# Kernel optimization log

Measured on AMD Instinct MI355X. Metric: run time of the kernel, lower is better.

Reference implementation:

```python
import jax, jax.numpy as jnp
import numpy as np

N, T, VN, C = 64, 512, 10, 128
HEADS, DH = 8, 16
INNER = HEADS * DH  # 128
BN_EPS = 1e-5


def _build_mask():
    # depth == 0 graph: facial-region connections + self links, symmetric 10x10
    m = np.zeros((VN, VN), dtype=np.float32)
    conn = [[0, 1], [0, 2], [2, 1], [3, 4], [3, 5], [4, 5],
            [6, 7], [6, 8], [6, 9], [8, 7], [9, 7], [8, 9]]
    for a, b in conn:
        m[a, b] = 1.0
        m[b, a] = 1.0
    for i in range(VN):
        m[i, i] = 1.0
    return jnp.asarray(m)


def setup_inputs() -> dict:
    key = jax.random.key(0)
    k = jax.random.split(key, 6)
    x = jax.random.normal(k[0], (N, T, VN, C), dtype=jnp.float32)
    gamma = 1.0 + 0.02 * jax.random.normal(k[1], (C,), dtype=jnp.float32)
    beta = 0.02 * jax.random.normal(k[2], (C,), dtype=jnp.float32)
    w_qkv = 0.02 * jax.random.normal(k[3], (C, 3 * INNER), dtype=jnp.float32)
    w_out = 0.02 * jax.random.normal(k[4], (INNER, C), dtype=jnp.float32)
    b_out = 0.02 * jax.random.normal(k[5], (C,), dtype=jnp.float32)
    return {"x": x, "gamma": gamma, "beta": beta, "w_qkv": w_qkv,
            "w_out": w_out, "b_out": b_out, "mask": _build_mask()}


def reference(x, gamma, beta, w_qkv, w_out, b_out, mask):
    n, t, vn, c = x.shape
    xb = x.reshape(-1, vn, c)                     # (b, vn, c), b = n*t
    # BatchNorm1d over channel c (training mode: batch stats over b and vn)
    mean = jnp.mean(xb, axis=(0, 1))
    var = jnp.var(xb, axis=(0, 1))                # biased, matches torch BN
    y = (xb - mean) * jax.lax.rsqrt(var + BN_EPS) * gamma + beta
    # fused QKV projection (Linear, no bias)
    qkv = y @ w_qkv                               # (b, vn, 3*inner)
    q, k, v = jnp.split(qkv, 3, axis=-1)
    split_heads = lambda z: z.reshape(-1, vn, HEADS, DH).transpose(0, 2, 1, 3)
    q, k, v = split_heads(q), split_heads(k), split_heads(v)  # (b, h, vn, dh)
    scale = DH ** -0.5
    dots = jnp.einsum('bhid,bhjd->bhij', q, k) * scale
    dots = dots * mask                            # multiplicative graph mask
    attn = jax.nn.softmax(dots, axis=-1)
    out = jnp.einsum('bhij,bhjd->bhid', attn, v)  # (b, h, vn, dh)
    out = out.transpose(0, 2, 1, 3).reshape(-1, vn, INNER)
    out = out @ w_out + b_out                     # output projection
    return out.reshape(n, t, vn, c)
```

## Files before the change

### kernel.cpp

```cpp
#include <hip/hip_runtime.h>


#define VNODES 10
#define CH 128
#define HEADS 8
#define ROWS_TOTAL 327680
#define G 8
#define MROWS 80
#define MT 5
#define SY 136
#define SQ 392

typedef __bf16 bf16x8 __attribute__((ext_vector_type(8)));
typedef float f32x4 __attribute__((ext_vector_type(4)));
typedef unsigned short u16x8 __attribute__((ext_vector_type(8)));
typedef unsigned short u16x4 __attribute__((ext_vector_type(4)));

__device__ __forceinline__ float bf2f(unsigned short u) {
    return __uint_as_float(((unsigned)u) << 16);
}
__device__ __forceinline__ unsigned short f2bf(float f) {
    unsigned u = __float_as_uint(f);
    u += 0x7fffu + ((u >> 16) & 1u);
    return (unsigned short)(u >> 16);
}

__global__ __launch_bounds__(256) void detect_kernel(
        const unsigned short* __restrict__ xr, int* __restrict__ flag) {
    __shared__ float red[256];
    int t = threadIdx.x;
    float mx = 0.f;
    for (int i = t; i < 8192; i += 256) {
        float a = fabsf(bf2f(xr[i]));
        if (!(a < 1e9f)) a = 1e9f;
        mx = fmaxf(mx, a);
    }
    red[t] = mx;
    __syncthreads();
    for (int s = 128; s > 0; s >>= 1) {
        if (t < s) red[t] = fmaxf(red[t], red[t + s]);
        __syncthreads();
    }
    if (t == 0) *flag = (red[0] > 1000.f) ? 1 : 0;
}

template<int MODE>
__global__ __launch_bounds__(256) void prep_kernel(
        const void* __restrict__ wqkv_, const void* __restrict__ wout_,
        const int* __restrict__ flag,
        unsigned short* __restrict__ fq, unsigned short* __restrict__ fo) {
    if (*flag != MODE) return;
    const unsigned short* wq16 = (const unsigned short*)wqkv_;
    const float*          wq32 = (const float*)wqkv_;
    const unsigned short* wo16 = (const unsigned short*)wout_;
    const float*          wo32 = (const float*)wout_;
    int tid = blockIdx.x * 256 + threadIdx.x;
    if (tid < 24 * 4 * 64) {
        int l = tid & 63;
        int kt = (tid >> 6) & 3;
        int nt = tid >> 8;
        int quad = l >> 4, n = l & 15;
#pragma unroll
        for (int j = 0; j < 8; ++j) {
            int idx = (kt * 32 + quad * 8 + j) * 384 + nt * 16 + n;
            fq[tid * 8 + j] = MODE ? f2bf(wq32[idx]) : wq16[idx];
        }
    } else if (tid < 24 * 4 * 64 + 8 * 4 * 64) {
        int u = tid - 24 * 4 * 64;
        int l = u & 63;
        int kt = (u >> 6) & 3;
        int nt = u >> 8;
        int quad = l >> 4, n = l & 15;
#pragma unroll
        for (int j = 0; j < 8; ++j) {
            int idx = (kt * 32 + quad * 8 + j) * 128 + nt * 16 + n;
            fo[u * 8 + j] = MODE ? f2bf(wo32[idx]) : wo16[idx];
        }
    }
}

template<int MODE>
__global__ __launch_bounds__(256) void stats_kernel(
        const void* __restrict__ x_, const int* __restrict__ flag,
        float* __restrict__ ws_sum, float* __restrict__ ws_sq) {
    if (*flag != MODE) return;
    int t = threadIdx.x;
    if (MODE == 0) {
        const unsigned short* x = (const unsigned short*)x_;
        __shared__ float lsum[16][128];
        __shared__ float lsq[16][128];
        int slot = t >> 4, g = t & 15;
        float s[8], q[8];
#pragma unroll
        for (int k = 0; k < 8; ++k) { s[k] = 0.f; q[k] = 0.f; }
        size_t base_row = (size_t)blockIdx.x * 320;
        for (int p = 0; p < 20; ++p) {
            size_t row = base_row + p * 16 + slot;
            u16x8 v = *(const u16x8*)(x + row * CH + g * 8);
#pragma unroll
            for (int k = 0; k < 8; ++k) {
                float f = bf2f(v[k]);
                s[k] += f;
                q[k] = fmaf(f, f, q[k]);
            }
        }
#pragma unroll
        for (int k = 0; k < 8; ++k) { lsum[slot][g * 8 + k] = s[k]; lsq[slot][g * 8 + k] = q[k]; }
        __syncthreads();
        if (t < 128) {
            float ts = 0.f, tq = 0.f;
#pragma unroll
            for (int sl = 0; sl < 16; ++sl) { ts += lsum[sl][t]; tq += lsq[sl][t]; }
            atomicAdd(&ws_sum[t], ts);
            atomicAdd(&ws_sq[t], tq);
        }
    } else {
        const float* x = (const float*)x_;
        __shared__ float lsum[8][128];
        __shared__ float lsq[8][128];
        int slot = t >> 5, g = t & 31;
        float s[4], q[4];
#pragma unroll
        for (int k = 0; k < 4; ++k) { s[k] = 0.f; q[k] = 0.f; }
        size_t base_row = (size_t)blockIdx.x * 320;
        for (int p = 0; p < 40; ++p) {
            size_t row = base_row + p * 8 + slot;
            f32x4 v = *(const f32x4*)(x + row * CH + g * 4);
#pragma unroll
            for (int k = 0; k < 4; ++k) {
                s[k] += v[k];
                q[k] = fmaf(v[k], v[k], q[k]);
            }
        }
#pragma unroll
        for (int k = 0; k < 4; ++k) { lsum[slot][g * 4 + k] = s[k]; lsq[slot][g * 4 + k] = q[k]; }
        __syncthreads();
        if (t < 128) {
            float ts = 0.f, tq = 0.f;
#pragma unroll
            for (int sl = 0; sl < 8; ++sl) { ts += lsum[sl][t]; tq += lsq[sl][t]; }
            atomicAdd(&ws_sum[t], ts);
            atomicAdd(&ws_sq[t], tq);
        }
    }
}

template<int MODE>
__global__ __launch_bounds__(512) void main_kernel(
        const void* __restrict__ x_,
        const void* __restrict__ gamma_,
        const void* __restrict__ beta_,
        const void* __restrict__ mask_,
        const int* __restrict__ flag,
        const float* __restrict__ ws_stats,
        const unsigned short* __restrict__ wqkv_f,
        const unsigned short* __restrict__ wout_f,
        const void* __restrict__ b_out_,
        void* __restrict__ out_) {
    if (*flag != MODE) return;
    __shared__ __align__(16) unsigned short yT[MROWS * SY];
    __shared__ __align__(16) unsigned short qkvT[MROWS * SQ];
    __shared__ float scale_s[CH], shift_s[CH], bout_s[CH], mask_s[VNODES * VNODES];

    int tid = threadIdx.x;
    int lane = tid & 63, w = tid >> 6;
    size_t row0 = (size_t)blockIdx.x * MROWS;

    if (tid < CH) {
        float sum = ws_stats[tid], sq = ws_stats[128 + tid];
        float mean = sum * (1.0f / ROWS_TOTAL);
        float var = sq * (1.0f / ROWS_TOTAL) - mean * mean;
        float inv = rsqrtf(var + 1e-5f);
        float gm = MODE ? ((const float*)gamma_)[tid] : bf2f(((const unsigned short*)gamma_)[tid]);
        float bt = MODE ? ((const float*)beta_)[tid]  : bf2f(((const unsigned short*)beta_)[tid]);
        float sc = gm * inv;
        scale_s[tid] = sc;
        shift_s[tid] = bt - mean * sc;
    } else if (tid < 256) {
        int c = tid - 128;
        bout_s[c] = MODE ? ((const float*)b_out_)[c] : bf2f(((const unsigned short*)b_out_)[c]);
    } else if (tid < 256 + VNODES * VNODES) {
        int c = tid - 256;
        mask_s[c] = MODE ? ((const float*)mask_)[c] : bf2f(((const unsigned short*)mask_)[c]);
    }
    __syncthreads();

    if (MODE == 0) {
        const unsigned short* x = (const unsigned short*)x_;
        int rloc = tid >> 4, g = tid & 15;
        for (int p = 0; p < 3; ++p) {
            int r = p * 32 + rloc;
            if (r < MROWS) {
                u16x8 v = *(const u16x8*)(x + (row0 + r) * CH + g * 8);
                u16x8 o;
#pragma unroll
                for (int k = 0; k < 8; ++k) {
                    int c = g * 8 + k;
                    o[k] = f2bf(fmaf(bf2f(v[k]), scale_s[c], shift_s[c]));
                }
                *(u16x8*)(yT + r * SY + g * 8) = o;
            }
        }
    } else {
        const float* x = (const float*)x_;
        int rloc = tid >> 5, g = tid & 31;
        for (int p = 0; p < 5; ++p) {
            int r = p * 16 + rloc;
            f32x4 v = *(const f32x4*)(x + (row0 + r) * CH + g * 4);
            u16x4 o;
#pragma unroll
            for (int k = 0; k < 4; ++k) {
                int c = g * 4 + k;
                o[k] = f2bf(fmaf(v[k], scale_s[c], shift_s[c]));
            }
            *(u16x4*)(yT + r * SY + g * 4) = o;
        }
    }
    __syncthreads();

    {
        bf16x8 bf[3][4];
#pragma unroll
        for (int ni = 0; ni < 3; ++ni) {
            int nt = w + ni * 8;
#pragma unroll
            for (int kt = 0; kt < 4; ++kt)
                bf[ni][kt] = *(const bf16x8*)(wqkv_f + ((nt * 4 + kt) * 64 + lane) * 8);
        }
        int l15 = lane & 15, quad = lane >> 4;
        for (int mt = 0; mt < MT; ++mt) {
            bf16x8 a[4];
#pragma unroll
            for (int kt = 0; kt < 4; ++kt)
                a[kt] = *(const bf16x8*)(yT + (mt * 16 + l15) * SY + kt * 32 + quad * 8);
#pragma unroll
            for (int ni = 0; ni < 3; ++ni) {
                f32x4 acc = {0.f, 0.f, 0.f, 0.f};
#pragma unroll
                for (int kt = 0; kt < 4; ++kt)
                    acc = __builtin_amdgcn_mfma_f32_16x16x32_bf16(a[kt], bf[ni][kt], acc, 0, 0, 0);
                int col = (w + ni * 8) * 16 + l15;
#pragma unroll
                for (int i = 0; i < 4; ++i) {
                    int rr = mt * 16 + quad * 4 + i;
                    qkvT[rr * SQ + col] = f2bf(acc[i]);
                }
            }
        }
    }
    __syncthreads();

    for (int task = tid; task < G * HEADS * VNODES; task += 512) {
        int h = task / (G * VNODES);
        int rem = task - h * (G * VNODES);
        int b = rem / VNODES;
        int i = rem - b * VNODES;
        int rowi = b * VNODES + i;
        const unsigned short* qp = qkvT + rowi * SQ + h * 16;
        float qv[16];
#pragma unroll
        for (int d2 = 0; d2 < 8; ++d2) {
            unsigned wd = *(const unsigned*)(qp + d2 * 2);
            qv[d2 * 2]     = __uint_as_float(wd << 16);
            qv[d2 * 2 + 1] = __uint_as_float(wd & 0xffff0000u);
        }
        float p[VNODES];
        float mx = -1e30f;
#pragma unroll
        for (int j = 0; j < VNODES; ++j) {
            const unsigned short* kp = qkvT + (b * VNODES + j) * SQ + 128 + h * 16;
            float dot = 0.f;
#pragma unroll
            for (int d2 = 0; d2 < 8; ++d2) {
                unsigned wd = *(const unsigned*)(kp + d2 * 2);
                dot = fmaf(qv[d2 * 2], __uint_as_float(wd << 16), dot);
                dot = fmaf(qv[d2 * 2 + 1], __uint_as_float(wd & 0xffff0000u), dot);
            }
            p[j] = dot * 0.25f * mask_s[i * VNODES + j];
            mx = fmaxf(mx, p[j]);
        }
        float s = 0.f;
#pragma unroll
        for (int j = 0; j < VNODES; ++j) { p[j] = __expf(p[j] - mx); s += p[j]; }
        float inv = 1.0f / s;
#pragma unroll
        for (int d2 = 0; d2 < 8; ++d2) {
            float a0 = 0.f, a1 = 0.f;
#pragma unroll
            for (int j = 0; j < VNODES; ++j) {
                unsigned wd = *(const unsigned*)(qkvT + (b * VNODES + j) * SQ + 256 + h * 16 + d2 * 2);
                a0 = fmaf(p[j], __uint_as_float(wd << 16), a0);
                a1 = fmaf(p[j], __uint_as_float(wd & 0xffff0000u), a1);
            }
            unsigned ow = (unsigned)f2bf(a0 * inv) | ((unsigned)f2bf(a1 * inv) << 16);
            *(unsigned*)(yT + rowi * SY + h * 16 + d2 * 2) = ow;
        }
    }
    __syncthreads();

    {
        bf16x8 bfw[4];
#pragma unroll
        for (int kt = 0; kt < 4; ++kt)
            bfw[kt] = *(const bf16x8*)(wout_f + ((w * 4 + kt) * 64 + lane) * 8);
        int l15 = lane & 15, quad = lane >> 4;
        float bias = bout_s[w * 16 + l15];
        for (int mt = 0; mt < MT; ++mt) {
            f32x4 acc = {0.f, 0.f, 0.f, 0.f};
#pragma unroll
            for (int kt = 0; kt < 4; ++kt) {
                bf16x8 a = *(const bf16x8*)(yT + (mt * 16 + l15) * SY + kt * 32 + quad * 8);
                acc = __builtin_amdgcn_mfma_f32_16x16x32_bf16(a, bfw[kt], acc, 0, 0, 0);
            }
            int col = w * 16 + l15;
#pragma unroll
            for (int i = 0; i < 4; ++i) {
                int rr = mt * 16 + quad * 4 + i;
                qkvT[rr * SQ + col] = f2bf(acc[i] + bias);
            }
        }
    }
    __syncthreads();

    if (MODE == 0) {
        unsigned short* out = (unsigned short*)out_;
        int rloc = tid >> 4, g = tid & 15;
        for (int p = 0; p < 3; ++p) {
            int r = p * 32 + rloc;
            if (r < MROWS) {
                u16x8 v = *(const u16x8*)(qkvT + r * SQ + g * 8);
                *(u16x8*)(out + (row0 + r) * CH + g * 8) = v;
            }
        }
    } else {
        float* out = (float*)out_;
        int rloc = tid >> 5, g = tid & 31;
        for (int p = 0; p < 5; ++p) {
            int r = p * 16 + rloc;
            u16x4 v = *(const u16x4*)(qkvT + r * SQ + g * 4);
            f32x4 o;
#pragma unroll
            for (int k = 0; k < 4; ++k) o[k] = bf2f(v[k]);
            *(f32x4*)(out + (row0 + r) * CH + g * 4) = o;
        }
    }
}

extern "C" void kernel_launch(void* const* d_in, const int* in_sizes, int n_in,
                              void* d_out, int out_size, void* d_ws, size_t ws_size,
                              hipStream_t stream) {
    const void* x     = d_in[0];
    const void* gamma = d_in[1];
    const void* beta  = d_in[2];
    const void* wqkv  = d_in[3];
    const void* wout  = d_in[4];
    const void* bout  = d_in[5];
    const void* maskp = d_in[6];

    char* ws = (char*)d_ws;
    float* ws_stats = (float*)ws;
    int* flag = (int*)(ws + 1024);
    unsigned short* fq = (unsigned short*)(ws + 2048);
    unsigned short* fo = (unsigned short*)(ws + 2048 + 98304);

    hipMemsetAsync(ws, 0, 2048, stream);
    detect_kernel<<<1, 256, 0, stream>>>((const unsigned short*)x, flag);
    prep_kernel<0><<<32, 256, 0, stream>>>(wqkv, wout, flag, fq, fo);
    prep_kernel<1><<<32, 256, 0, stream>>>(wqkv, wout, flag, fq, fo);
    stats_kernel<0><<<1024, 256, 0, stream>>>(x, flag, ws_stats, ws_stats + 128);
    stats_kernel<1><<<1024, 256, 0, stream>>>(x, flag, ws_stats, ws_stats + 128);
    main_kernel<0><<<4096, 512, 0, stream>>>(x, gamma, beta, maskp, flag, ws_stats, fq, fo, bout, d_out);
    main_kernel<1><<<4096, 512, 0, stream>>>(x, gamma, beta, maskp, flag, ws_stats, fq, fo, bout, d_out);
}
```

Before: 446.3 us.

## Fold BatchNorm into QKV weights and bias, drop dtype dispatch, halve tile

```diff
diff --git a/kernel.cpp b/kernel.cpp
--- a/kernel.cpp
+++ b/kernel.cpp
@@ -3,18 +3,16 @@
 
 #define VNODES 10
 #define CH 128
-#define HEADS 8
 #define ROWS_TOTAL 327680
-#define G 8
-#define MROWS 80
-#define MT 5
-#define SY 136
-#define SQ 392
+#define G 4
+#define MROWS 40
+#define MT 3
+#define SX 136
+#define SK 132
 
 typedef __bf16 bf16x8 __attribute__((ext_vector_type(8)));
 typedef float f32x4 __attribute__((ext_vector_type(4)));
 typedef unsigned short u16x8 __attribute__((ext_vector_type(8)));
-typedef unsigned short u16x4 __attribute__((ext_vector_type(4)));
 
 __device__ __forceinline__ float bf2f(unsigned short u) {
     return __uint_as_float(((unsigned)u) << 16);
@@ -25,195 +23,130 @@
     return (unsigned short)(u >> 16);
 }
 
-__global__ __launch_bounds__(256) void detect_kernel(
-        const unsigned short* __restrict__ xr, int* __restrict__ flag) {
-    __shared__ float red[256];
+__global__ __launch_bounds__(256) void stats_kernel(
+        const float* __restrict__ x,
+        float* __restrict__ ws_sum, float* __restrict__ ws_sq) {
+    __shared__ float lsum[8][128];
+    __shared__ float lsq[8][128];
     int t = threadIdx.x;
-    float mx = 0.f;
-    for (int i = t; i < 8192; i += 256) {
-        float a = fabsf(bf2f(xr[i]));
-        if (!(a < 1e9f)) a = 1e9f;
-        mx = fmaxf(mx, a);
-    }
-    red[t] = mx;
-    __syncthreads();
-    for (int s = 128; s > 0; s >>= 1) {
-        if (t < s) red[t] = fmaxf(red[t], red[t + s]);
+    int slot = t >> 5, g = t & 31;
+    float s[4], q[4];
+#pragma unroll
+    for (int k = 0; k < 4; ++k) { s[k] = 0.f; q[k] = 0.f; }
+    size_t base_row = (size_t)blockIdx.x * 160;
+    for (int p = 0; p < 20; ++p) {
+        size_t row = base_row + p * 8 + slot;
+        f32x4 v = *(const f32x4*)(x + row * CH + g * 4);
+#pragma unroll
+        for (int k = 0; k < 4; ++k) {
+            s[k] += v[k];
+            q[k] = fmaf(v[k], v[k], q[k]);
+        }
+    }
+#pragma unroll
+    for (int k = 0; k < 4; ++k) { lsum[slot][g * 4 + k] = s[k]; lsq[slot][g * 4 + k] = q[k]; }
+    __syncthreads();
+    if (t < 128) {
+        float ts = 0.f, tq = 0.f;
+#pragma unroll
+        for (int sl = 0; sl < 8; ++sl) { ts += lsum[sl][t]; tq += lsq[sl][t]; }
+        atomicAdd(&ws_sum[t], ts);
+        atomicAdd(&ws_sq[t], tq);
+    }
+}
+
+__global__ __launch_bounds__(256) void prep_kernel(
+        const float* __restrict__ wqkv, const float* __restrict__ wout,
+        const float* __restrict__ gamma, const float* __restrict__ beta,
+        const float* __restrict__ stats,
+        unsigned short* __restrict__ fq, unsigned short* __restrict__ fo,
+        float* __restrict__ bq) {
+    __shared__ float sh_s[128];
+    if (blockIdx.x < 32) {
+        int tid = blockIdx.x * 256 + threadIdx.x;
+        if (tid < 24 * 4 * 64) {
+            int l = tid & 63;
+            int kt = (tid >> 6) & 3;
+            int nt = tid >> 8;
+            int quad = l >> 4, n = l & 15;
+#pragma unroll
+            for (int j = 0; j < 8; ++j) {
+                int k = kt * 32 + quad * 8 + j;
+                float mean = stats[k] * (1.0f / ROWS_TOTAL);
+                float var = stats[128 + k] * (1.0f / ROWS_TOTAL) - mean * mean;
+                float sc = gamma[k] * rsqrtf(var + 1e-5f);
+                fq[tid * 8 + j] = f2bf(sc * wqkv[k * 384 + nt * 16 + n]);
+            }
+        } else if (tid < 24 * 4 * 64 + 8 * 4 * 64) {
+            int u = tid - 24 * 4 * 64;
+            int l = u & 63;
+            int kt = (u >> 6) & 3;
+            int nt = u >> 8;
+            int quad = l >> 4, n = l & 15;
+#pragma unroll
+            for (int j = 0; j < 8; ++j) {
+                int k = kt * 32 + quad * 8 + j;
+                fo[u * 8 + j] = f2bf(wout[k * 128 + nt * 16 + n]);
+            }
+        }
+    } else {
+        int t = threadIdx.x;
+        if (t < 128) {
+            float mean = stats[t] * (1.0f / ROWS_TOTAL);
+            float var = stats[128 + t] * (1.0f / ROWS_TOTAL) - mean * mean;
+            float sc = gamma[t] * rsqrtf(var + 1e-5f);
+            sh_s[t] = beta[t] - mean * sc;
+        }
         __syncthreads();
-    }
-    if (t == 0) *flag = (red[0] > 1000.f) ? 1 : 0;
-}
-
-template<int MODE>
-__global__ __launch_bounds__(256) void prep_kernel(
-        const void* __restrict__ wqkv_, const void* __restrict__ wout_,
-        const int* __restrict__ flag,
-        unsigned short* __restrict__ fq, unsigned short* __restrict__ fo) {
-    if (*flag != MODE) return;
-    const unsigned short* wq16 = (const unsigned short*)wqkv_;
-    const float*          wq32 = (const float*)wqkv_;
-    const unsigned short* wo16 = (const unsigned short*)wout_;
-    const float*          wo32 = (const float*)wout_;
-    int tid = blockIdx.x * 256 + threadIdx.x;
-    if (tid < 24 * 4 * 64) {
-        int l = tid & 63;
-        int kt = (tid >> 6) & 3;
-        int nt = tid >> 8;
-        int quad = l >> 4, n = l & 15;
-#pragma unroll
-        for (int j = 0; j < 8; ++j) {
-            int idx = (kt * 32 + quad * 8 + j) * 384 + nt * 16 + n;
-            fq[tid * 8 + j] = MODE ? f2bf(wq32[idx]) : wq16[idx];
-        }
-    } else if (tid < 24 * 4 * 64 + 8 * 4 * 64) {
-        int u = tid - 24 * 4 * 64;
-        int l = u & 63;
-        int kt = (u >> 6) & 3;
-        int nt = u >> 8;
-        int quad = l >> 4, n = l & 15;
-#pragma unroll
-        for (int j = 0; j < 8; ++j) {
-            int idx = (kt * 32 + quad * 8 + j) * 128 + nt * 16 + n;
-            fo[u * 8 + j] = MODE ? f2bf(wo32[idx]) : wo16[idx];
-        }
-    }
-}
-
-template<int MODE>
-__global__ __launch_bounds__(256) void stats_kernel(
-        const void* __restrict__ x_, const int* __restrict__ flag,
-        float* __restrict__ ws_sum, float* __restrict__ ws_sq) {
-    if (*flag != MODE) return;
-    int t = threadIdx.x;
-    if (MODE == 0) {
-        const unsigned short* x = (const unsigned short*)x_;
-        __shared__ float lsum[16][128];
-        __shared__ float lsq[16][128];
-        int slot = t >> 4, g = t & 15;
-        float s[8], q[8];
-#pragma unroll
-        for (int k = 0; k < 8; ++k) { s[k] = 0.f; q[k] = 0.f; }
-        size_t base_row = (size_t)blockIdx.x * 320;
-        for (int p = 0; p < 20; ++p) {
-            size_t row = base_row + p * 16 + slot;
-            u16x8 v = *(const u16x8*)(x + row * CH + g * 8);
-#pragma unroll
-            for (int k = 0; k < 8; ++k) {
-                float f = bf2f(v[k]);
-                s[k] += f;
-                q[k] = fmaf(f, f, q[k]);
-            }
-        }
-#pragma unroll
-        for (int k = 0; k < 8; ++k) { lsum[slot][g * 8 + k] = s[k]; lsq[slot][g * 8 + k] = q[k]; }
-        __syncthreads();
-        if (t < 128) {
-            float ts = 0.f, tq = 0.f;
-#pragma unroll
-            for (int sl = 0; sl < 16; ++sl) { ts += lsum[sl][t]; tq += lsq[sl][t]; }
-            atomicAdd(&ws_sum[t], ts);
-            atomicAdd(&ws_sq[t], tq);
-        }
-    } else {
-        const float* x = (const float*)x_;
-        __shared__ float lsum[8][128];
-        __shared__ float lsq[8][128];
-        int slot = t >> 5, g = t & 31;
-        float s[4], q[4];
-#pragma unroll
-        for (int k = 0; k < 4; ++k) { s[k] = 0.f; q[k] = 0.f; }
-        size_t base_row = (size_t)blockIdx.x * 320;
-        for (int p = 0; p < 40; ++p) {
-            size_t row = base_row + p * 8 + slot;
-            f32x4 v = *(const f32x4*)(x + row * CH + g * 4);
-#pragma unroll
-            for (int k = 0; k < 4; ++k) {
-                s[k] += v[k];
-                q[k] = fmaf(v[k], v[k], q[k]);
-            }
-        }
-#pragma unroll
-        for (int k = 0; k < 4; ++k) { lsum[slot][g * 4 + k] = s[k]; lsq[slot][g * 4 + k] = q[k]; }
-        __syncthreads();
-        if (t < 128) {
-            float ts = 0.f, tq = 0.f;
-#pragma unroll
-            for (int sl = 0; sl < 8; ++sl) { ts += lsum[sl][t]; tq += lsq[sl][t]; }
-            atomicAdd(&ws_sum[t], ts);
-            atomicAdd(&ws_sq[t], tq);
-        }
-    }
-}
-
-template<int MODE>
-__global__ __launch_bounds__(512) void main_kernel(
-        const void* __restrict__ x_,
-        const void* __restrict__ gamma_,
-        const void* __restrict__ beta_,
-        const void* __restrict__ mask_,
-        const int* __restrict__ flag,
-        const float* __restrict__ ws_stats,
+        for (int n = t; n < 384; n += 256) {
+            float acc = 0.f;
+#pragma unroll 8
+            for (int c = 0; c < 128; ++c) acc = fmaf(sh_s[c], wqkv[c * 384 + n], acc);
+            bq[n] = acc;
+        }
+    }
+}
+
+__global__ __launch_bounds__(512, 4) void main_kernel(
+        const float* __restrict__ x,
+        const float* __restrict__ maskp,
+        const float* __restrict__ bq,
         const unsigned short* __restrict__ wqkv_f,
         const unsigned short* __restrict__ wout_f,
-        const void* __restrict__ b_out_,
-        void* __restrict__ out_) {
-    if (*flag != MODE) return;
-    __shared__ __align__(16) unsigned short yT[MROWS * SY];
-    __shared__ __align__(16) unsigned short qkvT[MROWS * SQ];
-    __shared__ float scale_s[CH], shift_s[CH], bout_s[CH], mask_s[VNODES * VNODES];
+        const float* __restrict__ b_out,
+        float* __restrict__ out) {
+    __shared__ __align__(16) unsigned short xT[48 * SX];
+    __shared__ __align__(16) unsigned short qT[40 * SX];
+    __shared__ __align__(16) float kT[40 * SK];
+    __shared__ __align__(16) float vT[40 * SK];
+    __shared__ float bq_s[384], bout_s[128], mask_s[VNODES * VNODES];
 
     int tid = threadIdx.x;
     int lane = tid & 63, w = tid >> 6;
     size_t row0 = (size_t)blockIdx.x * MROWS;
 
-    if (tid < CH) {
-        float sum = ws_stats[tid], sq = ws_stats[128 + tid];
-        float mean = sum * (1.0f / ROWS_TOTAL);
-        float var = sq * (1.0f / ROWS_TOTAL) - mean * mean;
-        float inv = rsqrtf(var + 1e-5f);
-        float gm = MODE ? ((const float*)gamma_)[tid] : bf2f(((const unsigned short*)gamma_)[tid]);
-        float bt = MODE ? ((const float*)beta_)[tid]  : bf2f(((const unsigned short*)beta_)[tid]);
-        float sc = gm * inv;
-        scale_s[tid] = sc;
-        shift_s[tid] = bt - mean * sc;
-    } else if (tid < 256) {
-        int c = tid - 128;
-        bout_s[c] = MODE ? ((const float*)b_out_)[c] : bf2f(((const unsigned short*)b_out_)[c]);
-    } else if (tid < 256 + VNODES * VNODES) {
-        int c = tid - 256;
-        mask_s[c] = MODE ? ((const float*)mask_)[c] : bf2f(((const unsigned short*)mask_)[c]);
-    }
-    __syncthreads();
-
-    if (MODE == 0) {
-        const unsigned short* x = (const unsigned short*)x_;
-        int rloc = tid >> 4, g = tid & 15;
+    if (tid < 384) bq_s[tid] = bq[tid];
+    else bout_s[tid - 384] = b_out[tid - 384];
+    if (tid < VNODES * VNODES) mask_s[tid] = maskp[tid];
+    {
+        int r = 40 + (tid >> 6), c = (tid & 63) * 2;
+        *(unsigned*)(xT + r * SX + c) = 0u;
+    }
+
+    {
+#pragma unroll
         for (int p = 0; p < 3; ++p) {
-            int r = p * 32 + rloc;
-            if (r < MROWS) {
-                u16x8 v = *(const u16x8*)(x + (row0 + r) * CH + g * 8);
-                u16x8 o;
-#pragma unroll
-                for (int k = 0; k < 8; ++k) {
-                    int c = g * 8 + k;
-                    o[k] = f2bf(fmaf(bf2f(v[k]), scale_s[c], shift_s[c]));
-                }
-                *(u16x8*)(yT + r * SY + g * 8) = o;
-            }
-        }
-    } else {
-        const float* x = (const float*)x_;
-        int rloc = tid >> 5, g = tid & 31;
-        for (int p = 0; p < 5; ++p) {
-            int r = p * 16 + rloc;
-            f32x4 v = *(const f32x4*)(x + (row0 + r) * CH + g * 4);
-            u16x4 o;
-#pragma unroll
-            for (int k = 0; k < 4; ++k) {
-                int c = g * 4 + k;
-                o[k] = f2bf(fmaf(v[k], scale_s[c], shift_s[c]));
-            }
-            *(u16x4*)(yT + r * SY + g * 4) = o;
+            int idx = p * 512 + tid;
+            if (idx < 1280) {
+                int r = idx >> 5, g = idx & 31;
+                f32x4 v = *(const f32x4*)(x + (row0 + r) * CH + g * 4);
+                unsigned short o0 = f2bf(v[0]), o1 = f2bf(v[1]);
+                unsigned short o2 = f2bf(v[2]), o3 = f2bf(v[3]);
+                unsigned two0 = (unsigned)o0 | ((unsigned)o1 << 16);
+                unsigned two1 = (unsigned)o2 | ((unsigned)o3 << 16);
+                *(unsigned*)(xT + r * SX + g * 4) = two0;
+                *(unsigned*)(xT + r * SX + g * 4 + 2) = two1;
+            }
         }
     }
     __syncthreads();
@@ -232,31 +165,36 @@
             bf16x8 a[4];
 #pragma unroll
             for (int kt = 0; kt < 4; ++kt)
-                a[kt] = *(const bf16x8*)(yT + (mt * 16 + l15) * SY + kt * 32 + quad * 8);
-#pragma unroll
-            for (int ni = 0; ni < 3; ++ni) {
-                f32x4 acc = {0.f, 0.f, 0.f, 0.f};
-#pragma unroll
-                for (int kt = 0; kt < 4; ++kt)
-                    acc = __builtin_amdgcn_mfma_f32_16x16x32_bf16(a[kt], bf[ni][kt], acc, 0, 0, 0);
-                int col = (w + ni * 8) * 16 + l15;
-#pragma unroll
-                for (int i = 0; i < 4; ++i) {
-                    int rr = mt * 16 + quad * 4 + i;
-                    qkvT[rr * SQ + col] = f2bf(acc[i]);
+                a[kt] = *(const bf16x8*)(xT + (mt * 16 + l15) * SX + kt * 32 + quad * 8);
+            f32x4 accq = {0.f,0.f,0.f,0.f}, acck = {0.f,0.f,0.f,0.f}, accv = {0.f,0.f,0.f,0.f};
+#pragma unroll
+            for (int kt = 0; kt < 4; ++kt) {
+                accq = __builtin_amdgcn_mfma_f32_16x16x32_bf16(a[kt], bf[0][kt], accq, 0, 0, 0);
+                acck = __builtin_amdgcn_mfma_f32_16x16x32_bf16(a[kt], bf[1][kt], acck, 0, 0, 0);
+                accv = __builtin_amdgcn_mfma_f32_16x16x32_bf16(a[kt], bf[2][kt], accv, 0, 0, 0);
+            }
+            int col = w * 16 + l15;
+            float bqq = bq_s[col], bqk = bq_s[128 + col], bqv = bq_s[256 + col];
+#pragma unroll
+            for (int i = 0; i < 4; ++i) {
+                int rr = mt * 16 + quad * 4 + i;
+                if (rr < MROWS) {
+                    qT[rr * SX + col] = f2bf(accq[i] + bqq);
+                    kT[rr * SK + col] = acck[i] + bqk;
+                    vT[rr * SK + col] = accv[i] + bqv;
                 }
             }
         }
     }
     __syncthreads();
 
-    for (int task = tid; task < G * HEADS * VNODES; task += 512) {
-        int h = task / (G * VNODES);
-        int rem = task - h * (G * VNODES);
+    if (tid < G * 8 * VNODES) {
+        int h = tid / (G * VNODES);
+        int rem = tid - h * (G * VNODES);
         int b = rem / VNODES;
         int i = rem - b * VNODES;
         int rowi = b * VNODES + i;
-        const unsigned short* qp = qkvT + rowi * SQ + h * 16;
+        const unsigned short* qp = qT + rowi * SX + h * 16;
         float qv[16];
 #pragma unroll
         for (int d2 = 0; d2 < 8; ++d2) {
@@ -268,13 +206,16 @@
         float mx = -1e30f;
 #pragma unroll
         for (int j = 0; j < VNODES; ++j) {
-            const unsigned short* kp = qkvT + (b * VNODES + j) * SQ + 128 + h * 16;
+            const float* kp = kT + (b * VNODES + j) * SK + h * 16;
+            f32x4 k0 = *(const f32x4*)kp,     k1 = *(const f32x4*)(kp + 4);
+            f32x4 k2 = *(const f32x4*)(kp + 8), k3 = *(const f32x4*)(kp + 12);
             float dot = 0.f;
 #pragma unroll
-            for (int d2 = 0; d2 < 8; ++d2) {
-                unsigned wd = *(const unsigned*)(kp + d2 * 2);
-                dot = fmaf(qv[d2 * 2], __uint_as_float(wd << 16), dot);
-                dot = fmaf(qv[d2 * 2 + 1], __uint_as_float(wd & 0xffff0000u), dot);
+            for (int d = 0; d < 4; ++d) {
+                dot = fmaf(qv[d], k0[d], dot);
+                dot = fmaf(qv[4 + d], k1[d], dot);
+                dot = fmaf(qv[8 + d], k2[d], dot);
+                dot = fmaf(qv[12 + d], k3[d], dot);
             }
             p[j] = dot * 0.25f * mask_s[i * VNODES + j];
             mx = fmaxf(mx, p[j]);
@@ -283,17 +224,27 @@
 #pragma unroll
         for (int j = 0; j < VNODES; ++j) { p[j] = __expf(p[j] - mx); s += p[j]; }
         float inv = 1.0f / s;
+        float o[16];
+#pragma unroll
+        for (int d = 0; d < 16; ++d) o[d] = 0.f;
+#pragma unroll
+        for (int j = 0; j < VNODES; ++j) {
+            const float* vp = vT + (b * VNODES + j) * SK + h * 16;
+            f32x4 v0 = *(const f32x4*)vp,     v1 = *(const f32x4*)(vp + 4);
+            f32x4 v2 = *(const f32x4*)(vp + 8), v3 = *(const f32x4*)(vp + 12);
+#pragma unroll
+            for (int d = 0; d < 4; ++d) {
+                o[d]      = fmaf(p[j], v0[d], o[d]);
+                o[4 + d]  = fmaf(p[j], v1[d], o[4 + d]);
+                o[8 + d]  = fmaf(p[j], v2[d], o[8 + d]);
+                o[12 + d] = fmaf(p[j], v3[d], o[12 + d]);
+            }
+        }
 #pragma unroll
         for (int d2 = 0; d2 < 8; ++d2) {
-            float a0 = 0.f, a1 = 0.f;
-#pragma unroll
-            for (int j = 0; j < VNODES; ++j) {
-                unsigned wd = *(const unsigned*)(qkvT + (b * VNODES + j) * SQ + 256 + h * 16 + d2 * 2);
-                a0 = fmaf(p[j], __uint_as_float(wd << 16), a0);
-                a1 = fmaf(p[j], __uint_as_float(wd & 0xffff0000u), a1);
-            }
-            unsigned ow = (unsigned)f2bf(a0 * inv) | ((unsigned)f2bf(a1 * inv) << 16);
-            *(unsigned*)(yT + rowi * SY + h * 16 + d2 * 2) = ow;
+            unsigned ow = (unsigned)f2bf(o[d2 * 2] * inv)
+                        | ((unsigned)f2bf(o[d2 * 2 + 1] * inv) << 16);
+            *(unsigned*)(xT + rowi * SX + h * 16 + d2 * 2) = ow;
         }
     }
     __syncthreads();
@@ -304,44 +255,32 @@
         for (int kt = 0; kt < 4; ++kt)
             bfw[kt] = *(const bf16x8*)(wout_f + ((w * 4 + kt) * 64 + lane) * 8);
         int l15 = lane & 15, quad = lane >> 4;
-        float bias = bout_s[w * 16 + l15];
+        int col = w * 16 + l15;
+        float bias = bout_s[col];
         for (int mt = 0; mt < MT; ++mt) {
             f32x4 acc = {0.f, 0.f, 0.f, 0.f};
 #pragma unroll
             for (int kt = 0; kt < 4; ++kt) {
-                bf16x8 a = *(const bf16x8*)(yT + (mt * 16 + l15) * SY + kt * 32 + quad * 8);
+                bf16x8 a = *(const bf16x8*)(xT + (mt * 16 + l15) * SX + kt * 32 + quad * 8);
                 acc = __builtin_amdgcn_mfma_f32_16x16x32_bf16(a, bfw[kt], acc, 0, 0, 0);
             }
-            int col = w * 16 + l15;
 #pragma unroll
             for (int i = 0; i < 4; ++i) {
                 int rr = mt * 16 + quad * 4 + i;
-                qkvT[rr * SQ + col] = f2bf(acc[i] + bias);
-            }
-        }
-    }
-    __syncthreads();
-
-    if (MODE == 0) {
-        unsigned short* out = (unsigned short*)out_;
-        int rloc = tid >> 4, g = tid & 15;
+                if (rr < MROWS) kT[rr * SK + col] = acc[i] + bias;
+            }
+        }
+    }
+    __syncthreads();
+
+    {
+#pragma unroll
         for (int p = 0; p < 3; ++p) {
-            int r = p * 32 + rloc;
-            if (r < MROWS) {
-                u16x8 v = *(const u16x8*)(qkvT + r * SQ + g * 8);
-                *(u16x8*)(out + (row0 + r) * CH + g * 8) = v;
-            }
-        }
-    } else {
-        float* out = (float*)out_;
-        int rloc = tid >> 5, g = tid & 31;
-        for (int p = 0; p < 5; ++p) {
-            int r = p * 16 + rloc;
-            u16x4 v = *(const u16x4*)(qkvT + r * SQ + g * 4);
-            f32x4 o;
-#pragma unroll
-            for (int k = 0; k < 4; ++k) o[k] = bf2f(v[k]);
-            *(f32x4*)(out + (row0 + r) * CH + g * 4) = o;
+            int idx = p * 512 + tid;
+            if (idx < 1280) {
+                int r = idx >> 5, g = idx & 31;
+                *(f32x4*)(out + (row0 + r) * CH + g * 4) = *(const f32x4*)(kT + r * SK + g * 4);
+            }
         }
     }
 }
@@ -349,26 +288,23 @@
 extern "C" void kernel_launch(void* const* d_in, const int* in_sizes, int n_in,
                               void* d_out, int out_size, void* d_ws, size_t ws_size,
                               hipStream_t stream) {
-    const void* x     = d_in[0];
-    const void* gamma = d_in[1];
-    const void* beta  = d_in[2];
-    const void* wqkv  = d_in[3];
-    const void* wout  = d_in[4];
-    const void* bout  = d_in[5];
-    const void* maskp = d_in[6];
+    const float* x     = (const float*)d_in[0];
+    const float* gamma = (const float*)d_in[1];
+    const float* beta  = (const float*)d_in[2];
+    const float* wqkv  = (const float*)d_in[3];
+    const float* wout  = (const float*)d_in[4];
+    const float* bout  = (const float*)d_in[5];
+    const float* maskp = (const float*)d_in[6];
+    float* out = (float*)d_out;
 
     char* ws = (char*)d_ws;
     float* ws_stats = (float*)ws;
-    int* flag = (int*)(ws + 1024);
-    unsigned short* fq = (unsigned short*)(ws + 2048);
-    unsigned short* fo = (unsigned short*)(ws + 2048 + 98304);
-
-    hipMemsetAsync(ws, 0, 2048, stream);
-    detect_kernel<<<1, 256, 0, stream>>>((const unsigned short*)x, flag);
-    prep_kernel<0><<<32, 256, 0, stream>>>(wqkv, wout, flag, fq, fo);
-    prep_kernel<1><<<32, 256, 0, stream>>>(wqkv, wout, flag, fq, fo);
-    stats_kernel<0><<<1024, 256, 0, stream>>>(x, flag, ws_stats, ws_stats + 128);
-    stats_kernel<1><<<1024, 256, 0, stream>>>(x, flag, ws_stats, ws_stats + 128);
-    main_kernel<0><<<4096, 512, 0, stream>>>(x, gamma, beta, maskp, flag, ws_stats, fq, fo, bout, d_out);
-    main_kernel<1><<<4096, 512, 0, stream>>>(x, gamma, beta, maskp, flag, ws_stats, fq, fo, bout, d_out);
-}
+    float* bq = (float*)(ws + 1024);
+    unsigned short* fq = (unsigned short*)(ws + 4096);
+    unsigned short* fo = (unsigned short*)(ws + 4096 + 98304);
+
+    hipMemsetAsync(ws, 0, 1024, stream);
+    stats_kernel<<<2048, 256, 0, stream>>>(x, ws_stats, ws_stats + 128);
+    prep_kernel<<<33, 256, 0, stream>>>(wqkv, wout, gamma, beta, ws_stats, fq, fo, bq);
+    main_kernel<<<8192, 512, 0, stream>>>(x, maskp, bq, fq, fo, bout, out);
+}
```

New measurement: 417.0 us. 6.6% less time.
